# Kernel optimization log

Measured on AMD Instinct MI355X. Metric: run time of the kernel, lower is better.

Reference implementation:

```python
import math
import jax, jax.numpy as jnp
import numpy as np


def setup_inputs() -> dict:
    key = jax.random.key(0)
    k1, k2, k3 = jax.random.split(key, 3)
    B, T, D = 4, 2048, 2048
    x = jax.random.normal(k1, (B, T, D), dtype=jnp.float32)
    w_qkv = jax.random.normal(k2, (D, 3 * D), dtype=jnp.float32) * 0.02
    w_proj = jax.random.normal(k3, (D, D), dtype=jnp.float32) * 0.02
    b_proj = jnp.zeros((D,), dtype=jnp.float32)
    return {"x": x, "w_qkv": w_qkv, "w_proj": w_proj, "b_proj": b_proj, "n_head": 16}


def reference(x, w_qkv, w_proj, b_proj, n_head):
    B, T, D = x.shape
    N = n_head
    H = D // N
    qkv = x @ w_qkv                       # (B,T,3D)
    q, k, v = jnp.split(qkv, 3, axis=-1)  # each (B,T,D)
    # NOTE: original torch code does .view(B, n_head, T, H) directly on the
    # (B,T,D) tensor (a raw memory reinterpretation, not a head split+transpose).
    q = q.reshape(B, N, T, H)
    k = k.reshape(B, N, T, H)
    v = v.reshape(B, N, T, H)
    # full T x T score matrix, scaled by sqrt(D) (not sqrt(H)) as in the original
    a = jnp.einsum('bnih,bnjh->bnij', q, k) / math.sqrt(D)  # (B,N,T,T)
    a = jax.nn.softmax(a, axis=3)
    # torch.einsum('bntt,bnth->bnth', a, v): repeated 't' in first operand
    # takes the DIAGONAL of the attention matrix, then elementwise-scales v.
    diag = jnp.diagonal(a, axis1=2, axis2=3)  # (B,N,T)
    o = diag[..., None] * v                   # (B,N,T,H)
    o = jnp.transpose(o, (0, 2, 1, 3)).reshape(B, T, D)
    return o @ w_proj + b_proj
```

## Files before the change

### kernel.cpp

```cpp
#include <hip/hip_runtime.h>
#include <hip/hip_bf16.h>

typedef short bf16x8 __attribute__((ext_vector_type(8)));
typedef float f32x4 __attribute__((ext_vector_type(4)));

__device__ __forceinline__ unsigned short f2bf(float f) {
  union { float f; unsigned int u; } x; x.f = f;
  return (unsigned short)((x.u + 0x7fffu + ((x.u >> 16) & 1u)) >> 16);
}
__device__ __forceinline__ float bf2f(unsigned short u) {
  union { unsigned int u; float f; } x; x.u = ((unsigned int)u) << 16;
  return x.f;
}
__device__ __forceinline__ void gload_lds16(const void* g, void* l) {
  __builtin_amdgcn_global_load_lds((const __attribute__((address_space(1))) void*)g,
                                   (__attribute__((address_space(3))) void*)l, 16, 0, 0);
}

__global__ void cast_f32_bf16(const float* __restrict__ src, unsigned short* __restrict__ dst) {
  int i = blockIdx.x * blockDim.x + threadIdx.x;
  float4 v = reinterpret_cast<const float4*>(src)[i];
  ushort4 o;
  o.x = f2bf(v.x); o.y = f2bf(v.y); o.z = f2bf(v.z); o.w = f2bf(v.w);
  reinterpret_cast<ushort4*>(dst)[i] = o;
}

__global__ void transpose_cast(const float* __restrict__ src, unsigned short* __restrict__ dst,
                               int R, int C) {
  __shared__ float tile[32][33];
  int c0 = blockIdx.x * 32, r0 = blockIdx.y * 32;
  int tx = threadIdx.x, ty = threadIdx.y;
#pragma unroll
  for (int i = 0; i < 4; ++i)
    tile[ty + i * 8][tx] = src[(size_t)(r0 + ty + i * 8) * C + (c0 + tx)];
  __syncthreads();
#pragma unroll
  for (int i = 0; i < 4; ++i)
    dst[(size_t)(c0 + ty + i * 8) * R + (r0 + tx)] = f2bf(tile[tx][ty + i * 8]);
}

template <int EPI>
__global__ __launch_bounds__(512, 2)
void gemm256(const unsigned short* __restrict__ A, const unsigned short* __restrict__ Bt,
             unsigned short* __restrict__ Qo, unsigned short* __restrict__ Ko,
             unsigned short* __restrict__ Vo, float* __restrict__ Cf,
             const float* __restrict__ bias, int M, int N, int K) {
  extern __shared__ __align__(16) char lds[];
  const int tid = threadIdx.x;
  const int lane = tid & 63, wid = tid >> 6;
  const int wm = wid >> 2, wn = wid & 3;
  const int fr = lane & 15, fq = lane >> 4;

  const int nbn = N >> 8;
  const int cpx = gridDim.x >> 3;
  const int id = blockIdx.x;
  const int sw = (id & 7) * cpx + (id >> 3);
  const int bm = sw / nbn, bn = sw % nbn;
  const int row0 = bm << 8, col0 = bn << 8;

  const int NT = K >> 6;

  const int srow = tid >> 3;
  const int scol = ((tid & 7) ^ (srow & 7)) << 3;

  auto stage = [&](int j, int slot) {
    if (j < 4 * NT) {
      const int t = j >> 2, ht = j & 3;
      const int isB = (ht == 1 || ht == 2);
      const int h = (ht >= 2) ? 1 : 0;
      const unsigned short* base = isB ? Bt : A;
      const int grow = (isB ? col0 : row0) + h * 128 + srow;
      const unsigned short* src = base + (size_t)grow * K + t * 64 + scol;
      char* l0 = lds + slot * 16384 + tid * 16;
      gload_lds16(src, l0);
      gload_lds16(src + (size_t)64 * K, l0 + 8192);
    } else {
      char* l0 = lds + 7 * 16384 + tid * 16;
      gload_lds16(A + (tid << 3), l0);
      gload_lds16(A + (tid << 3), l0 + 8192);
    }
  };

  f32x4 acc[2][4][2][2] = {};

  stage(0, 0); stage(1, 1); stage(2, 2); stage(3, 3); stage(4, 4);
  asm volatile("s_waitcnt vmcnt(6)" ::: "memory");
  asm volatile("s_barrier" ::: "memory");

  int sA0 = 0, sB0 = 1, sB1 = 2, sA1 = 3, sst = 5;

  for (int k = 0; k < NT; ++k) {
    const int j0 = 4 * k + 5;
    bf16x8 a[4][2], b0[2][2], b1[2][2];

    {
      const char* Ab = lds + sA0 * 16384;
      const char* Bb = lds + sB0 * 16384;
#pragma unroll
      for (int i2 = 0; i2 < 4; ++i2)
#pragma unroll
        for (int ks = 0; ks < 2; ++ks) {
          const int byte = ((((wm * 4 + i2) * 16 + fr) * 128) + ks * 64 + fq * 16) ^ ((fr & 7) << 4);
          a[i2][ks] = *reinterpret_cast<const bf16x8*>(Ab + byte);
        }
#pragma unroll
      for (int j2 = 0; j2 < 2; ++j2)
#pragma unroll
        for (int ks = 0; ks < 2; ++ks) {
          const int byte = ((((wn * 2 + j2) * 16 + fr) * 128) + ks * 64 + fq * 16) ^ ((fr & 7) << 4);
          b0[j2][ks] = *reinterpret_cast<const bf16x8*>(Bb + byte);
        }
      stage(j0 + 0, sst); sst = (sst == 6) ? 0 : sst + 1;
      asm volatile("s_waitcnt vmcnt(6)" ::: "memory");
      asm volatile("s_barrier" ::: "memory");
      __builtin_amdgcn_s_setprio(1);
#pragma unroll
      for (int i2 = 0; i2 < 4; ++i2)
#pragma unroll
        for (int j2 = 0; j2 < 2; ++j2)
#pragma unroll
          for (int ks = 0; ks < 2; ++ks)
            acc[0][i2][0][j2] =
                __builtin_amdgcn_mfma_f32_16x16x32_bf16(a[i2][ks], b0[j2][ks], acc[0][i2][0][j2], 0, 0, 0);
      __builtin_amdgcn_s_setprio(0);
    }

    {
      const char* Bb = lds + sB1 * 16384;
#pragma unroll
      for (int j2 = 0; j2 < 2; ++j2)
#pragma unroll
        for (int ks = 0; ks < 2; ++ks) {
          const int byte = ((((wn * 2 + j2) * 16 + fr) * 128) + ks * 64 + fq * 16) ^ ((fr & 7) << 4);
          b1[j2][ks] = *reinterpret_cast<const bf16x8*>(Bb + byte);
        }
      stage(j0 + 1, sst); sst = (sst == 6) ? 0 : sst + 1;
      asm volatile("s_waitcnt vmcnt(6)" ::: "memory");
      asm volatile("s_barrier" ::: "memory");
      __builtin_amdgcn_s_setprio(1);
#pragma unroll
      for (int i2 = 0; i2 < 4; ++i2)
#pragma unroll
        for (int j2 = 0; j2 < 2; ++j2)
#pragma unroll
          for (int ks = 0; ks < 2; ++ks)
            acc[0][i2][1][j2] =
                __builtin_amdgcn_mfma_f32_16x16x32_bf16(a[i2][ks], b1[j2][ks], acc[0][i2][1][j2], 0, 0, 0);
      __builtin_amdgcn_s_setprio(0);
    }

    {
      const char* Ab = lds + sA1 * 16384;
#pragma unroll
      for (int i2 = 0; i2 < 4; ++i2)
#pragma unroll
        for (int ks = 0; ks < 2; ++ks) {
          const int byte = ((((wm * 4 + i2) * 16 + fr) * 128) + ks * 64 + fq * 16) ^ ((fr & 7) << 4);
          a[i2][ks] = *reinterpret_cast<const bf16x8*>(Ab + byte);
        }
      stage(j0 + 2, sst); sst = (sst == 6) ? 0 : sst + 1;
      asm volatile("s_waitcnt vmcnt(6)" ::: "memory");
      asm volatile("s_barrier" ::: "memory");
      __builtin_amdgcn_s_setprio(1);
#pragma unroll
      for (int i2 = 0; i2 < 4; ++i2)
#pragma unroll
        for (int j2 = 0; j2 < 2; ++j2)
#pragma unroll
          for (int ks = 0; ks < 2; ++ks)
            acc[1][i2][0][j2] =
                __builtin_amdgcn_mfma_f32_16x16x32_bf16(a[i2][ks], b0[j2][ks], acc[1][i2][0][j2], 0, 0, 0);
      __builtin_amdgcn_s_setprio(0);
    }

    {
      stage(j0 + 3, sst); sst = (sst == 6) ? 0 : sst + 1;
      asm volatile("s_waitcnt vmcnt(6)" ::: "memory");
      asm volatile("s_barrier" ::: "memory");
      __builtin_amdgcn_s_setprio(1);
#pragma unroll
      for (int i2 = 0; i2 < 4; ++i2)
#pragma unroll
        for (int j2 = 0; j2 < 2; ++j2)
#pragma unroll
          for (int ks = 0; ks < 2; ++ks)
            acc[1][i2][1][j2] =
                __builtin_amdgcn_mfma_f32_16x16x32_bf16(a[i2][ks], b1[j2][ks], acc[1][i2][1][j2], 0, 0, 0);
      __builtin_amdgcn_s_setprio(0);
    }

    sA0 += 4; if (sA0 >= 7) sA0 -= 7;
    sB0 += 4; if (sB0 >= 7) sB0 -= 7;
    sB1 += 4; if (sB1 >= 7) sB1 -= 7;
    sA1 += 4; if (sA1 >= 7) sA1 -= 7;
  }

  asm volatile("s_waitcnt vmcnt(0)" ::: "memory");

#pragma unroll
  for (int mh = 0; mh < 2; ++mh)
#pragma unroll
    for (int i2 = 0; i2 < 4; ++i2) {
      const int rbase = row0 + (mh * 8 + wm * 4 + i2) * 16 + fq * 4;
#pragma unroll
      for (int nh = 0; nh < 2; ++nh)
#pragma unroll
        for (int j2 = 0; j2 < 2; ++j2) {
          const int col = col0 + (nh * 8 + wn * 2 + j2) * 16 + fr;
#pragma unroll
          for (int r = 0; r < 4; ++r) {
            const float v = acc[mh][i2][nh][j2][r];
            const int row = rbase + r;
            if (EPI == 0) {
              const int seg = col >> 11, cc = col & 2047;
              unsigned short* dst = (seg == 0) ? Qo : (seg == 1 ? Ko : Vo);
              dst[(size_t)row * 2048 + cc] = f2bf(v);
            } else {
              Cf[(size_t)row * N + col] = v + bias[col];
            }
          }
        }
    }
}

__global__ __launch_bounds__(256, 2)
void attn_diag_ov(const unsigned short* __restrict__ Q, const unsigned short* __restrict__ K,
                  const unsigned short* __restrict__ V, unsigned short* __restrict__ OV) {
  __shared__ __align__(16) unsigned short qs[64 * 128];
  __shared__ __align__(16) unsigned short ks[128 * 128];
  __shared__ float dlds[64];
  const int tid = threadIdx.x;
  const int lane = tid & 63, wid = tid >> 6;
  const int head = blockIdx.y;
  const int b = head >> 4, n = head & 15;
  const int t0 = blockIdx.x << 6;
  const size_t hoff = (size_t)head << 18;
  const unsigned short* Qh = Q + hoff;
  const unsigned short* Kh = K + hoff;
  const unsigned short* Vh = V + hoff;

  const char* qsrc = (const char*)(Qh + ((size_t)t0 << 7));
#pragma unroll
  for (int i = 0; i < 4; ++i) {
    const int fb = (i * 256 + tid) << 4;
    const int sb = fb ^ (((fb >> 8) & 7) << 4);
    gload_lds16(qsrc + sb, (char*)qs + fb);
  }

  const int fr = lane & 15;
  const int fkb = (lane >> 4) << 4;
  const int g4 = (lane >> 4) << 2;

  float rsum[4] = {0.f, 0.f, 0.f, 0.f};
  float dnum[4] = {0.f, 0.f, 0.f, 0.f};
  const float scale = 0.02209708691207961f;
  bf16x8 afrag[4];

  for (int jc = 0; jc < 2048; jc += 128) {
    const char* ksrc = (const char*)(Kh + ((size_t)jc << 7));
#pragma unroll
    for (int i = 0; i < 8; ++i) {
      const int fb = (i * 256 + tid) << 4;
      const int sb = fb ^ (((fb >> 8) & 7) << 4);
      gload_lds16(ksrc + sb, (char*)ks + fb);
    }
    __syncthreads();
    if (jc == 0) {
#pragma unroll
      for (int kk = 0; kk < 4; ++kk) {
        const int row = wid * 16 + fr;
        const int byte = (row << 8) + (kk << 6) + fkb;
        afrag[kk] = *reinterpret_cast<const bf16x8*>((const char*)qs + (byte ^ ((row & 7) << 4)));
      }
    }
#pragma unroll
    for (int jt = 0; jt < 8; ++jt) {
      f32x4 acc = {0.f, 0.f, 0.f, 0.f};
#pragma unroll
      for (int kk = 0; kk < 4; ++kk) {
        const int row = jt * 16 + fr;
        const int byte = (row << 8) + (kk << 6) + fkb;
        bf16x8 bfrag = *reinterpret_cast<const bf16x8*>((const char*)ks + (byte ^ ((row & 7) << 4)));
        acc = __builtin_amdgcn_mfma_f32_16x16x32_bf16(afrag[kk], bfrag, acc, 0, 0, 0);
      }
      const int colj = jc + jt * 16 + fr;
      const int rowt = t0 + wid * 16 + g4;
#pragma unroll
      for (int r = 0; r < 4; ++r) {
        const float e = __expf(acc[r] * scale);
        rsum[r] += e;
        if (colj == rowt + r) dnum[r] = e;
      }
    }
    __syncthreads();
  }

#pragma unroll
  for (int r = 0; r < 4; ++r) {
#pragma unroll
    for (int s = 1; s < 16; s <<= 1) {
      rsum[r] += __shfl_xor(rsum[r], s, 64);
      dnum[r] += __shfl_xor(dnum[r], s, 64);
    }
  }
  if (fr == 0) {
#pragma unroll
    for (int r = 0; r < 4; ++r)
      dlds[wid * 16 + g4 + r] = dnum[r] / rsum[r];
  }
  __syncthreads();

  const unsigned short* vsrc = Vh + ((size_t)t0 << 7);
  unsigned short* dst = OV + ((size_t)((b << 11) + t0)) * 2048 + (n << 7);
#pragma unroll
  for (int c = 0; c < 4; ++c) {
    const int flat = (c * 256 + tid) << 3;
    const int row = flat >> 7, col = flat & 127;
    bf16x8 v = *reinterpret_cast<const bf16x8*>(vsrc + flat);
    const float d = dlds[row];
    bf16x8 o;
#pragma unroll
    for (int e = 0; e < 8; ++e)
      o[e] = (short)f2bf(bf2f((unsigned short)v[e]) * d);
    *reinterpret_cast<bf16x8*>(dst + (size_t)row * 2048 + col) = o;
  }
}

extern "C" void kernel_launch(void* const* d_in, const int* in_sizes, int n_in,
                              void* d_out, int out_size, void* d_ws, size_t ws_size,
                              hipStream_t stream) {
  const float* x = (const float*)d_in[0];
  const float* w_qkv = (const float*)d_in[1];
  const float* w_proj = (const float*)d_in[2];
  const float* b_proj = (const float*)d_in[3];
  float* out = (float*)d_out;

  char* p = (char*)d_ws;
  unsigned short* Xb = (unsigned short*)p;     p += (size_t)8192 * 2048 * 2;
  unsigned short* WqkvT = (unsigned short*)p;  p += (size_t)6144 * 2048 * 2;
  unsigned short* WprojT = (unsigned short*)p; p += (size_t)2048 * 2048 * 2;
  unsigned short* Qb = (unsigned short*)p;     p += (size_t)8192 * 2048 * 2;
  unsigned short* Kb = (unsigned short*)p;     p += (size_t)8192 * 2048 * 2;
  unsigned short* Vb = (unsigned short*)p;     p += (size_t)8192 * 2048 * 2;
  unsigned short* OV = (unsigned short*)p;     p += (size_t)8192 * 2048 * 2;

  (void)hipFuncSetAttribute((const void*)gemm256<0>,
                            hipFuncAttributeMaxDynamicSharedMemorySize, 131072);
  (void)hipFuncSetAttribute((const void*)gemm256<1>,
                            hipFuncAttributeMaxDynamicSharedMemorySize, 131072);

  cast_f32_bf16<<<16384, 256, 0, stream>>>(x, Xb);
  transpose_cast<<<dim3(192, 64), dim3(32, 8), 0, stream>>>(w_qkv, WqkvT, 2048, 6144);
  transpose_cast<<<dim3(64, 64), dim3(32, 8), 0, stream>>>(w_proj, WprojT, 2048, 2048);

  gemm256<0><<<dim3(32 * 24), 512, 131072, stream>>>(Xb, WqkvT, Qb, Kb, Vb, nullptr, nullptr,
                                                     8192, 6144, 2048);
  attn_diag_ov<<<dim3(32, 64), 256, 0, stream>>>(Qb, Kb, Vb, OV);
  gemm256<1><<<dim3(32 * 8), 512, 131072, stream>>>(OV, WprojT, nullptr, nullptr, nullptr, out,
                                                    b_proj, 8192, 2048, 2048);
}
```

Before: 393.5 us.

## Prefetch next LDS fragments into registers before each MFMA phase

Reorders the GEMM main loop so each phase reads the operand fragments for the following phase from LDS right after the barrier, then runs the current MFMAs. A second A-fragment register buffer (aA/aB) makes this register double-buffering possible. The aim is to hide LDS read latency behind matrix-core work instead of stalling on it at the start of each phase. The cost is extra VGPR pressure, plus a dependence on the slot rotation staying hazard-free with the async global-to-LDS staging.

New measurement: 569.7 us. 44.8% more time.

```diff
diff --git a/kernel.cpp b/kernel.cpp
--- a/kernel.cpp
+++ b/kernel.cpp
@@ -81,38 +81,44 @@
     }
   };
 
+  auto readA = [&](const char* base, bf16x8 (&dst)[4][2]) {
+#pragma unroll
+    for (int i2 = 0; i2 < 4; ++i2)
+#pragma unroll
+      for (int ks = 0; ks < 2; ++ks) {
+        const int byte = ((((wm * 4 + i2) * 16 + fr) * 128) + ks * 64 + fq * 16) ^ ((fr & 7) << 4);
+        dst[i2][ks] = *reinterpret_cast<const bf16x8*>(base + byte);
+      }
+  };
+  auto readB = [&](const char* base, bf16x8 (&dst)[2][2]) {
+#pragma unroll
+    for (int j2 = 0; j2 < 2; ++j2)
+#pragma unroll
+      for (int ks = 0; ks < 2; ++ks) {
+        const int byte = ((((wn * 2 + j2) * 16 + fr) * 128) + ks * 64 + fq * 16) ^ ((fr & 7) << 4);
+        dst[j2][ks] = *reinterpret_cast<const bf16x8*>(base + byte);
+      }
+  };
+
   f32x4 acc[2][4][2][2] = {};
+  bf16x8 aA[4][2], aB[4][2], b0[2][2], b1[2][2];
 
   stage(0, 0); stage(1, 1); stage(2, 2); stage(3, 3); stage(4, 4);
   asm volatile("s_waitcnt vmcnt(6)" ::: "memory");
   asm volatile("s_barrier" ::: "memory");
+  readA(lds + 0 * 16384, aA);
+  readB(lds + 1 * 16384, b0);
 
   int sA0 = 0, sB0 = 1, sB1 = 2, sA1 = 3, sst = 5;
 
   for (int k = 0; k < NT; ++k) {
     const int j0 = 4 * k + 5;
-    bf16x8 a[4][2], b0[2][2], b1[2][2];
 
     {
-      const char* Ab = lds + sA0 * 16384;
-      const char* Bb = lds + sB0 * 16384;
-#pragma unroll
-      for (int i2 = 0; i2 < 4; ++i2)
-#pragma unroll
-        for (int ks = 0; ks < 2; ++ks) {
-          const int byte = ((((wm * 4 + i2) * 16 + fr) * 128) + ks * 64 + fq * 16) ^ ((fr & 7) << 4);
-          a[i2][ks] = *reinterpret_cast<const bf16x8*>(Ab + byte);
-        }
-#pragma unroll
-      for (int j2 = 0; j2 < 2; ++j2)
-#pragma unroll
-        for (int ks = 0; ks < 2; ++ks) {
-          const int byte = ((((wn * 2 + j2) * 16 + fr) * 128) + ks * 64 + fq * 16) ^ ((fr & 7) << 4);
-          b0[j2][ks] = *reinterpret_cast<const bf16x8*>(Bb + byte);
-        }
       stage(j0 + 0, sst); sst = (sst == 6) ? 0 : sst + 1;
       asm volatile("s_waitcnt vmcnt(6)" ::: "memory");
       asm volatile("s_barrier" ::: "memory");
+      readB(lds + sB1 * 16384, b1);
       __builtin_amdgcn_s_setprio(1);
 #pragma unroll
       for (int i2 = 0; i2 < 4; ++i2)
@@ -121,22 +127,15 @@
 #pragma unroll
           for (int ks = 0; ks < 2; ++ks)
             acc[0][i2][0][j2] =
-                __builtin_amdgcn_mfma_f32_16x16x32_bf16(a[i2][ks], b0[j2][ks], acc[0][i2][0][j2], 0, 0, 0);
+                __builtin_amdgcn_mfma_f32_16x16x32_bf16(aA[i2][ks], b0[j2][ks], acc[0][i2][0][j2], 0, 0, 0);
       __builtin_amdgcn_s_setprio(0);
     }
 
     {
-      const char* Bb = lds + sB1 * 16384;
-#pragma unroll
-      for (int j2 = 0; j2 < 2; ++j2)
-#pragma unroll
-        for (int ks = 0; ks < 2; ++ks) {
-          const int byte = ((((wn * 2 + j2) * 16 + fr) * 128) + ks * 64 + fq * 16) ^ ((fr & 7) << 4);
-          b1[j2][ks] = *reinterpret_cast<const bf16x8*>(Bb + byte);
-        }
       stage(j0 + 1, sst); sst = (sst == 6) ? 0 : sst + 1;
       asm volatile("s_waitcnt vmcnt(6)" ::: "memory");
       asm volatile("s_barrier" ::: "memory");
+      readA(lds + sA1 * 16384, aB);
       __builtin_amdgcn_s_setprio(1);
 #pragma unroll
       for (int i2 = 0; i2 < 4; ++i2)
@@ -145,22 +144,16 @@
 #pragma unroll
           for (int ks = 0; ks < 2; ++ks)
             acc[0][i2][1][j2] =
-                __builtin_amdgcn_mfma_f32_16x16x32_bf16(a[i2][ks], b1[j2][ks], acc[0][i2][1][j2], 0, 0, 0);
+                __builtin_amdgcn_mfma_f32_16x16x32_bf16(aA[i2][ks], b1[j2][ks], acc[0][i2][1][j2], 0, 0, 0);
       __builtin_amdgcn_s_setprio(0);
     }
 
     {
-      const char* Ab = lds + sA1 * 16384;
-#pragma unroll
-      for (int i2 = 0; i2 < 4; ++i2)
-#pragma unroll
-        for (int ks = 0; ks < 2; ++ks) {
-          const int byte = ((((wm * 4 + i2) * 16 + fr) * 128) + ks * 64 + fq * 16) ^ ((fr & 7) << 4);
-          a[i2][ks] = *reinterpret_cast<const bf16x8*>(Ab + byte);
-        }
       stage(j0 + 2, sst); sst = (sst == 6) ? 0 : sst + 1;
       asm volatile("s_waitcnt vmcnt(6)" ::: "memory");
       asm volatile("s_barrier" ::: "memory");
+      int s = sA0 + 4; if (s >= 7) s -= 7;
+      readA(lds + s * 16384, aA);
       __builtin_amdgcn_s_setprio(1);
 #pragma unroll
       for (int i2 = 0; i2 < 4; ++i2)
@@ -169,7 +162,7 @@
 #pragma unroll
           for (int ks = 0; ks < 2; ++ks)
             acc[1][i2][0][j2] =
-                __builtin_amdgcn_mfma_f32_16x16x32_bf16(a[i2][ks], b0[j2][ks], acc[1][i2][0][j2], 0, 0, 0);
+                __builtin_amdgcn_mfma_f32_16x16x32_bf16(aB[i2][ks], b0[j2][ks], acc[1][i2][0][j2], 0, 0, 0);
       __builtin_amdgcn_s_setprio(0);
     }
 
@@ -177,6 +170,8 @@
       stage(j0 + 3, sst); sst = (sst == 6) ? 0 : sst + 1;
       asm volatile("s_waitcnt vmcnt(6)" ::: "memory");
       asm volatile("s_barrier" ::: "memory");
+      int s = sB0 + 4; if (s >= 7) s -= 7;
+      readB(lds + s * 16384, b0);
       __builtin_amdgcn_s_setprio(1);
 #pragma unroll
       for (int i2 = 0; i2 < 4; ++i2)
@@ -185,7 +180,7 @@
 #pragma unroll
           for (int ks = 0; ks < 2; ++ks)
             acc[1][i2][1][j2] =
-                __builtin_amdgcn_mfma_f32_16x16x32_bf16(a[i2][ks], b1[j2][ks], acc[1][i2][1][j2], 0, 0, 0);
+                __builtin_amdgcn_mfma_f32_16x16x32_bf16(aB[i2][ks], b1[j2][ks], acc[1][i2][1][j2], 0, 0, 0);
       __builtin_amdgcn_s_setprio(0);
     }
 
```

## Restructure diag-attention kernel with larger Q tiles and double-buffered K staging

Applied to the files above, without the earlier changes.

The attention-diagonal kernel now handles 256 query rows per 512-thread block, each wave holding two 16-row Q fragments in registers loaded straight from global memory. K chunks are double-buffered in LDS with a 16-way XOR swizzle, so the next chunk loads while the current one is computed. Each K fragment read from LDS now feeds two MFMA row tiles. The goal is to cut K reloads per query and hide global-load latency behind compute, at the cost of more registers and 64KB of LDS per block, which may limit occupancy.

Result: faster. 375.7 us (-4.5%).

```diff
diff --git a/kernel.cpp b/kernel.cpp
--- a/kernel.cpp
+++ b/kernel.cpp
@@ -223,105 +223,111 @@
     }
 }
 
-__global__ __launch_bounds__(256, 2)
+__global__ __launch_bounds__(512, 2)
 void attn_diag_ov(const unsigned short* __restrict__ Q, const unsigned short* __restrict__ K,
                   const unsigned short* __restrict__ V, unsigned short* __restrict__ OV) {
-  __shared__ __align__(16) unsigned short qs[64 * 128];
-  __shared__ __align__(16) unsigned short ks[128 * 128];
-  __shared__ float dlds[64];
+  __shared__ __align__(16) char ks[2][128 * 256];
+  __shared__ float dlds[256];
   const int tid = threadIdx.x;
   const int lane = tid & 63, wid = tid >> 6;
-  const int head = blockIdx.y;
+  const int d = blockIdx.x;
+  const int head = d & 63, tb = d >> 6;
   const int b = head >> 4, n = head & 15;
-  const int t0 = blockIdx.x << 6;
+  const int t0 = tb << 8;
   const size_t hoff = (size_t)head << 18;
   const unsigned short* Qh = Q + hoff;
   const unsigned short* Kh = K + hoff;
   const unsigned short* Vh = V + hoff;
 
-  const char* qsrc = (const char*)(Qh + ((size_t)t0 << 7));
-#pragma unroll
-  for (int i = 0; i < 4; ++i) {
-    const int fb = (i * 256 + tid) << 4;
-    const int sb = fb ^ (((fb >> 8) & 7) << 4);
-    gload_lds16(qsrc + sb, (char*)qs + fb);
-  }
-
-  const int fr = lane & 15;
-  const int fkb = (lane >> 4) << 4;
-  const int g4 = (lane >> 4) << 2;
-
-  float rsum[4] = {0.f, 0.f, 0.f, 0.f};
-  float dnum[4] = {0.f, 0.f, 0.f, 0.f};
+  const int fr = lane & 15, fq = lane >> 4;
+  const int g4 = fq << 2;
+  const int qrow0 = t0 + wid * 32;
+
+  bf16x8 qf[2][4];
+#pragma unroll
+  for (int m = 0; m < 2; ++m)
+#pragma unroll
+    for (int kk = 0; kk < 4; ++kk)
+      qf[m][kk] = *reinterpret_cast<const bf16x8*>(
+          Qh + (size_t)(qrow0 + m * 16 + fr) * 128 + kk * 32 + fq * 8);
+
+  auto stageK = [&](int jc, int s) {
+    const char* ksrc = (const char*)(Kh + ((size_t)jc << 7));
+#pragma unroll
+    for (int i = 0; i < 4; ++i) {
+      const int flat = i * 8192 + tid * 16;
+      const int row = flat >> 8, c = (flat >> 4) & 15;
+      const int sb = (row << 8) + ((c ^ (row & 15)) << 4);
+      gload_lds16(ksrc + sb, &ks[s][0] + flat);
+    }
+  };
+
+  float rsum[2][4] = {};
+  float dnum[2][4] = {};
   const float scale = 0.02209708691207961f;
-  bf16x8 afrag[4];
-
-  for (int jc = 0; jc < 2048; jc += 128) {
-    const char* ksrc = (const char*)(Kh + ((size_t)jc << 7));
-#pragma unroll
-    for (int i = 0; i < 8; ++i) {
-      const int fb = (i * 256 + tid) << 4;
-      const int sb = fb ^ (((fb >> 8) & 7) << 4);
-      gload_lds16(ksrc + sb, (char*)ks + fb);
-    }
-    __syncthreads();
-    if (jc == 0) {
-#pragma unroll
-      for (int kk = 0; kk < 4; ++kk) {
-        const int row = wid * 16 + fr;
-        const int byte = (row << 8) + (kk << 6) + fkb;
-        afrag[kk] = *reinterpret_cast<const bf16x8*>((const char*)qs + (byte ^ ((row & 7) << 4)));
-      }
-    }
+
+  stageK(0, 0);
+  asm volatile("s_waitcnt vmcnt(0)" ::: "memory");
+  asm volatile("s_barrier" ::: "memory");
+
+  for (int t = 0; t < 16; ++t) {
+    const int jc = t << 7;
+    if (t < 15) stageK(jc + 128, (t + 1) & 1);
+    const char* buf = &ks[t & 1][0];
 #pragma unroll
     for (int jt = 0; jt < 8; ++jt) {
-      f32x4 acc = {0.f, 0.f, 0.f, 0.f};
+      bf16x8 bfrag[4];
 #pragma unroll
       for (int kk = 0; kk < 4; ++kk) {
         const int row = jt * 16 + fr;
-        const int byte = (row << 8) + (kk << 6) + fkb;
-        bf16x8 bfrag = *reinterpret_cast<const bf16x8*>((const char*)ks + (byte ^ ((row & 7) << 4)));
-        acc = __builtin_amdgcn_mfma_f32_16x16x32_bf16(afrag[kk], bfrag, acc, 0, 0, 0);
+        const int s = kk * 4 + fq;
+        bfrag[kk] = *reinterpret_cast<const bf16x8*>(buf + (row << 8) + ((s ^ (row & 15)) << 4));
       }
-      const int colj = jc + jt * 16 + fr;
-      const int rowt = t0 + wid * 16 + g4;
-#pragma unroll
-      for (int r = 0; r < 4; ++r) {
-        const float e = __expf(acc[r] * scale);
-        rsum[r] += e;
-        if (colj == rowt + r) dnum[r] = e;
+#pragma unroll
+      for (int m = 0; m < 2; ++m) {
+        f32x4 acc = {0.f, 0.f, 0.f, 0.f};
+#pragma unroll
+        for (int kk = 0; kk < 4; ++kk)
+          acc = __builtin_amdgcn_mfma_f32_16x16x32_bf16(qf[m][kk], bfrag[kk], acc, 0, 0, 0);
+        const int colj = jc + jt * 16 + fr;
+        const int rowt = qrow0 + m * 16 + g4;
+#pragma unroll
+        for (int r = 0; r < 4; ++r) {
+          const float e = __expf(acc[r] * scale);
+          rsum[m][r] += e;
+          if (colj == rowt + r) dnum[m][r] = e;
+        }
       }
     }
-    __syncthreads();
+    asm volatile("s_waitcnt vmcnt(0)" ::: "memory");
+    asm volatile("s_barrier" ::: "memory");
   }
 
 #pragma unroll
-  for (int r = 0; r < 4; ++r) {
-#pragma unroll
-    for (int s = 1; s < 16; s <<= 1) {
-      rsum[r] += __shfl_xor(rsum[r], s, 64);
-      dnum[r] += __shfl_xor(dnum[r], s, 64);
-    }
-  }
-  if (fr == 0) {
-#pragma unroll
-    for (int r = 0; r < 4; ++r)
-      dlds[wid * 16 + g4 + r] = dnum[r] / rsum[r];
-  }
+  for (int m = 0; m < 2; ++m)
+#pragma unroll
+    for (int r = 0; r < 4; ++r) {
+#pragma unroll
+      for (int s = 1; s < 16; s <<= 1) {
+        rsum[m][r] += __shfl_xor(rsum[m][r], s, 64);
+        dnum[m][r] += __shfl_xor(dnum[m][r], s, 64);
+      }
+      if (fr == 0) dlds[wid * 32 + m * 16 + g4 + r] = dnum[m][r] / rsum[m][r];
+    }
   __syncthreads();
 
   const unsigned short* vsrc = Vh + ((size_t)t0 << 7);
   unsigned short* dst = OV + ((size_t)((b << 11) + t0)) * 2048 + (n << 7);
 #pragma unroll
-  for (int c = 0; c < 4; ++c) {
-    const int flat = (c * 256 + tid) << 3;
+  for (int c = 0; c < 8; ++c) {
+    const int flat = (c * 512 + tid) << 3;
     const int row = flat >> 7, col = flat & 127;
     bf16x8 v = *reinterpret_cast<const bf16x8*>(vsrc + flat);
-    const float d = dlds[row];
+    const float dd = dlds[row];
     bf16x8 o;
 #pragma unroll
     for (int e = 0; e < 8; ++e)
-      o[e] = (short)f2bf(bf2f((unsigned short)v[e]) * d);
+      o[e] = (short)f2bf(bf2f((unsigned short)v[e]) * dd);
     *reinterpret_cast<bf16x8*>(dst + (size_t)row * 2048 + col) = o;
   }
 }
@@ -355,7 +361,7 @@
 
   gemm256<0><<<dim3(32 * 24), 512, 131072, stream>>>(Xb, WqkvT, Qb, Kb, Vb, nullptr, nullptr,
                                                      8192, 6144, 2048);
-  attn_diag_ov<<<dim3(32, 64), 256, 0, stream>>>(Qb, Kb, Vb, OV);
+  attn_diag_ov<<<dim3(512), 512, 0, stream>>>(Qb, Kb, Vb, OV);
   gemm256<1><<<dim3(32 * 8), 512, 131072, stream>>>(OV, WprojT, nullptr, nullptr, nullptr, out,
                                                     b_proj, 8192, 2048, 2048);
 }
```
